# Optimization experiments

Hardware: AMD Instinct MI355X
Metric: run time of the kernel (lower is better)

The kernel has to match this reference:

```python
import jax, jax.numpy as jnp
import numpy as np

B, C, H, W = 8, 192, 128, 128
NH = 4  # num_heads
EPS = 1e-12


def setup_inputs() -> dict:
    key = jax.random.key(0)
    ks = jax.random.split(key, 10)
    s = 1.0 / np.sqrt(C)
    return {
        "x_q": jax.random.normal(ks[0], (B, C, H, W), jnp.float32),
        "x_k": jax.random.normal(ks[1], (B, C, H, W), jnp.float32),
        "Wq": jax.random.uniform(ks[2], (C, C), jnp.float32, -s, s),
        "bq": jax.random.uniform(ks[3], (C,), jnp.float32, -s, s),
        "Wkv": jax.random.uniform(ks[4], (2 * C, C), jnp.float32, -s, s),
        "bkv": jax.random.uniform(ks[5], (2 * C,), jnp.float32, -s, s),
        "Wp": jax.random.uniform(ks[6], (C, C), jnp.float32, -s, s),
        "bp": jax.random.uniform(ks[7], (C,), jnp.float32, -s, s),
        "temperature": jnp.ones((NH, 1, 1), jnp.float32),
    }


def _l2norm(x, axis):
    # torch F.normalize: x / clamp_min(||x||, eps)
    n = jnp.sqrt(jnp.sum(x * x, axis=axis, keepdims=True))
    return x / jnp.maximum(n, EPS)


def reference(x_q, x_k, Wq, bq, Wkv, bkv, Wp, bp, temperature):
    # 1x1 convs == channel matmuls
    q = jnp.einsum('oc,bchw->bohw', Wq, x_q) + bq[:, None, None]
    kv = jnp.einsum('oc,bchw->bohw', Wkv, x_k) + bkv[:, None, None]
    k, v = jnp.split(kv, 2, axis=1)

    def heads(t):  # (B,C,H,W) -> (B,NH,C//NH, H*W)
        return t.reshape(B, NH, C // NH, H * W)

    q, k, v = heads(q), heads(k), heads(v)
    q = _l2norm(q, 2)
    k = _l2norm(k, 2)

    attn_scale = 0.1 * jax.nn.sigmoid(temperature)  # (NH,1,1)
    attn = jnp.einsum('bhcd,bhkd->bhck', q, k) * attn_scale
    attn = jax.nn.softmax(attn, axis=-1)
    out = jnp.einsum('bhck,bhkd->bhcd', attn, v)
    out = out.reshape(B, C, H, W)
    out = jnp.einsum('oc,bchw->bohw', Wp, out) + bp[:, None, None]
    return out
```

## Files before the change

kernel.cpp:

```cpp
#include <hip/hip_runtime.h>
#include <hip/hip_bf16.h>

#define HW 16384
#define CC 192
#define BB 8
#define NHD 4
#define HD 48

typedef __attribute__((ext_vector_type(8))) short  short8;
typedef __attribute__((ext_vector_type(4))) float  f32x4;

static __device__ __forceinline__ unsigned short f2bf(float f) {
  unsigned u = __float_as_uint(f);
  u += 0x7fffu + ((u >> 16) & 1u);
  return (unsigned short)(u >> 16);
}
static __device__ __forceinline__ unsigned pk2bf(float lo, float hi) {
  __hip_bfloat162 h = __float22bfloat162_rn(make_float2(lo, hi));
  return *reinterpret_cast<unsigned*>(&h);
}

static __device__ __forceinline__ void ldsbar() {
  asm volatile("" ::: "memory");
  asm volatile("s_waitcnt lgkmcnt(0)" ::: "memory");
  __builtin_amdgcn_s_barrier();
  asm volatile("" ::: "memory");
}

__global__ __launch_bounds__(256) void cast_w_kernel(
    const float* __restrict__ Wq, const float* __restrict__ Wkv,
    unsigned short* __restrict__ Wb)
{
  const int i = blockIdx.x * 256 + threadIdx.x;
  const float v = (i < CC*CC) ? Wq[i] : Wkv[i - CC*CC];
  Wb[i] = f2bf(v);
}

__global__ __launch_bounds__(256, 2) void qkg_kernel(
    const float* __restrict__ x_q, const float* __restrict__ x_k,
    const unsigned short* __restrict__ wb,
    const float* __restrict__ bq, const float* __restrict__ bkv,
    float* __restrict__ gpart)
{
  const int tid  = threadIdx.x;
  const int lane = tid & 63;
  const int wv   = tid >> 6;
  const int b    = blockIdx.y;
  const int p0   = blockIdx.x * 256;
  const int l15  = lane & 15;
  const int lg   = lane >> 4;
  const int qd   = tid & 15;

  __shared__ unsigned short Xs[64][200];
  __shared__ unsigned short QN[NHD][48][68];
  __shared__ unsigned short KN[NHD][48][68];

  const float* Xq = x_q + (size_t)b*CC*HW;
  const float* Xk = x_k + (size_t)b*CC*HW;

  f32x4 pre[12];
  auto LOADT = [&](const float* X, int pb) {
    #pragma unroll
    for (int i = 0; i < 6; ++i) {
      const int cp = (tid >> 4) + i*16;
      const float* base = X + (size_t)(2*cp)*HW + pb + qd*4;
      pre[2*i]   = *(const f32x4*)(base);
      pre[2*i+1] = *(const f32x4*)(base + HW);
    }
  };
  auto WRITET = [&]() {
    #pragma unroll
    for (int i = 0; i < 6; ++i) {
      const int cp = (tid >> 4) + i*16;
      #pragma unroll
      for (int j = 0; j < 4; ++j)
        *(unsigned*)&Xs[qd*4 + j][2*cp] = pk2bf(pre[2*i][j], pre[2*i+1][j]);
    }
  };

  auto PROJ = [&](const unsigned short* W, const float* bias,
                  unsigned short (*DST)[68]) {
    f32x4 acc[3][4];
    #pragma unroll
    for (int mt = 0; mt < 3; ++mt)
      #pragma unroll
      for (int nt = 0; nt < 4; ++nt)
        acc[mt][nt] = (f32x4){0.f, 0.f, 0.f, 0.f};

    #pragma unroll
    for (int kk = 0; kk < 6; ++kk) {
      short8 afr[3], bfr[4];
      #pragma unroll
      for (int mt = 0; mt < 3; ++mt)
        afr[mt] = *(const short8*)(W + (size_t)(wv*48 + mt*16 + l15)*CC + kk*32 + lg*8);
      #pragma unroll
      for (int nt = 0; nt < 4; ++nt)
        bfr[nt] = *(const short8*)&Xs[nt*16 + l15][kk*32 + lg*8];
      #pragma unroll
      for (int mt = 0; mt < 3; ++mt)
        #pragma unroll
        for (int nt = 0; nt < 4; ++nt)
          acc[mt][nt] = __builtin_amdgcn_mfma_f32_16x16x32_bf16(
              afr[mt], bfr[nt], acc[mt][nt], 0, 0, 0);
    }

    #pragma unroll
    for (int nt = 0; nt < 4; ++nt) {
      float v[3][4];
      float ss = 0.f;
      #pragma unroll
      for (int mt = 0; mt < 3; ++mt)
        #pragma unroll
        for (int r = 0; r < 4; ++r) {
          const float x = acc[mt][nt][r] + bias[wv*48 + mt*16 + lg*4 + r];
          v[mt][r] = x;
          ss += x*x;
        }
      ss += __shfl_xor(ss, 16);
      ss += __shfl_xor(ss, 32);
      const float rn = 1.0f / fmaxf(sqrtf(ss), 1e-12f);
      #pragma unroll
      for (int mt = 0; mt < 3; ++mt)
        #pragma unroll
        for (int r = 0; r < 4; ++r)
          DST[mt*16 + lg*4 + r][nt*16 + l15] = f2bf(v[mt][r] * rn);
    }
  };

  f32x4 gacc[3][3];
  #pragma unroll
  for (int mt = 0; mt < 3; ++mt)
    #pragma unroll
    for (int nt = 0; nt < 3; ++nt)
      gacc[mt][nt] = (f32x4){0.f, 0.f, 0.f, 0.f};

  LOADT(Xq, p0);
  for (int t = 0; t < 4; ++t) {
    const int pb = p0 + t*64;
    WRITET();
    ldsbar();
    LOADT(Xk, pb);
    PROJ(wb, bq, QN[wv]);
    ldsbar();
    WRITET();
    ldsbar();
    if (t < 3) LOADT(Xq, pb + 64);
    PROJ(wb + (size_t)CC*CC, bkv, KN[wv]);
    ldsbar();

    #pragma unroll
    for (int s = 0; s < 2; ++s) {
      short8 ga[3], gb[3];
      #pragma unroll
      for (int mt = 0; mt < 3; ++mt)
        ga[mt] = *(const short8*)&QN[wv][mt*16 + l15][s*32 + lg*8];
      #pragma unroll
      for (int nt = 0; nt < 3; ++nt)
        gb[nt] = *(const short8*)&KN[wv][nt*16 + l15][s*32 + lg*8];
      #pragma unroll
      for (int mt = 0; mt < 3; ++mt)
        #pragma unroll
        for (int nt = 0; nt < 3; ++nt)
          gacc[mt][nt] = __builtin_amdgcn_mfma_f32_16x16x32_bf16(
              ga[mt], gb[nt], gacc[mt][nt], 0, 0, 0);
    }
  }

  float* G = gpart + ((size_t)(b*NHD + wv)*64 + blockIdx.x)*2304;
  #pragma unroll
  for (int mt = 0; mt < 3; ++mt)
    #pragma unroll
    for (int nt = 0; nt < 3; ++nt)
      #pragma unroll
      for (int r = 0; r < 4; ++r)
        G[(mt*16 + lg*4 + r)*HD + nt*16 + l15] = gacc[mt][nt][r];
}

__global__ __launch_bounds__(256) void proj_fin(
    const float* __restrict__ x_k,
    const unsigned short* __restrict__ w3b,
    const float* __restrict__ b3,
    float* __restrict__ of)
{
  const int tid  = threadIdx.x;
  const int lane = tid & 63;
  const int wv   = tid >> 6;
  const int b    = blockIdx.y;
  const int p0   = blockIdx.x * 256;
  const int l15  = lane & 15;
  const int lg   = lane >> 4;
  const int qd   = tid & 15;

  __shared__ unsigned short Xt[2][64][200];

  const float* X = x_k + (size_t)b*CC*HW;
  const unsigned short* Wb = w3b + (size_t)b*CC*CC;
  const float* bias = b3 + (size_t)b*CC;

  short8 afr[6][3];
  #pragma unroll
  for (int kk = 0; kk < 6; ++kk)
    #pragma unroll
    for (int mt = 0; mt < 3; ++mt)
      afr[kk][mt] = *(const short8*)(Wb + (size_t)(wv*48 + mt*16 + l15)*CC + kk*32 + lg*8);

  float bv[3][4];
  #pragma unroll
  for (int mt = 0; mt < 3; ++mt)
    #pragma unroll
    for (int r = 0; r < 4; ++r)
      bv[mt][r] = bias[wv*48 + mt*16 + lg*4 + r];

  f32x4 pre[12];
  auto LOADT = [&](int pb) {
    #pragma unroll
    for (int i = 0; i < 6; ++i) {
      const int cp = (tid >> 4) + i*16;
      const float* base = X + (size_t)(2*cp)*HW + pb + qd*4;
      pre[2*i]   = *(const f32x4*)(base);
      pre[2*i+1] = *(const f32x4*)(base + HW);
    }
  };
  auto WRITET = [&](int buf) {
    #pragma unroll
    for (int i = 0; i < 6; ++i) {
      const int cp = (tid >> 4) + i*16;
      #pragma unroll
      for (int j = 0; j < 4; ++j)
        *(unsigned*)&Xt[buf][qd*4 + j][2*cp] = pk2bf(pre[2*i][j], pre[2*i+1][j]);
    }
  };

  float* Ofp = of + (size_t)b*CC*HW;

  auto COMPUTE = [&](int buf, int pb) {
    f32x4 acc[3][4];
    #pragma unroll
    for (int mt = 0; mt < 3; ++mt)
      #pragma unroll
      for (int nt = 0; nt < 4; ++nt)
        acc[mt][nt] = (f32x4){0.f, 0.f, 0.f, 0.f};

    #pragma unroll
    for (int kk = 0; kk < 6; ++kk) {
      short8 bfr[4];
      #pragma unroll
      for (int nt = 0; nt < 4; ++nt)
        bfr[nt] = *(const short8*)&Xt[buf][nt*16 + l15][kk*32 + lg*8];
      #pragma unroll
      for (int mt = 0; mt < 3; ++mt)
        #pragma unroll
        for (int nt = 0; nt < 4; ++nt)
          acc[mt][nt] = __builtin_amdgcn_mfma_f32_16x16x32_bf16(
              afr[kk][mt], bfr[nt], acc[mt][nt], 0, 0, 0);
    }

    #pragma unroll
    for (int nt = 0; nt < 4; ++nt) {
      const int col = pb + nt*16 + l15;
      #pragma unroll
      for (int mt = 0; mt < 3; ++mt)
        #pragma unroll
        for (int r = 0; r < 4; ++r)
          Ofp[(size_t)(wv*48 + mt*16 + lg*4 + r)*HW + col] = acc[mt][nt][r] + bv[mt][r];
    }
  };

  LOADT(p0);
  WRITET(0);
  ldsbar();
  #pragma unroll
  for (int t = 0; t < 4; ++t) {
    if (t < 3) LOADT(p0 + (t+1)*64);
    COMPUTE(t & 1, p0 + t*64);
    if (t < 3) {
      WRITET((t & 1) ^ 1);
      ldsbar();
    }
  }
}

__global__ __launch_bounds__(256) void attn_m_kernel(
    const float* __restrict__ Gpart,
    const float* __restrict__ Wp,
    const float* __restrict__ temp,
    float* __restrict__ Mf)
{
  __shared__ float att[HD][52];
  const int bh  = blockIdx.x;
  const int b   = bh >> 2, h = bh & 3;
  const int tid = threadIdx.x;
  const float* src = Gpart + (size_t)bh*64*2304;

  #pragma unroll
  for (int i = 0; i < 9; ++i) {
    const int e = tid + i*256;
    float s = 0.f;
    #pragma unroll
    for (int k = 0; k < 64; ++k) s += src[(size_t)k*2304 + e];
    att[e/48][e%48] = s;
  }
  __syncthreads();

  const int g = tid >> 2, sl = tid & 3;
  if (g < HD) {
    const float t = temp[h];
    const float scale = 0.1f / (1.0f + expf(-t));
    float* row = att[g];
    float m = -1e30f;
    #pragma unroll
    for (int jj = 0; jj < 12; ++jj) m = fmaxf(m, row[sl + jj*4]);
    m = fmaxf(m, __shfl_xor(m, 1));
    m = fmaxf(m, __shfl_xor(m, 2));
    float ev[12];
    float s = 0.f;
    #pragma unroll
    for (int jj = 0; jj < 12; ++jj) {
      const float e = expf((row[sl + jj*4] - m) * scale);
      ev[jj] = e; s += e;
    }
    s += __shfl_xor(s, 1);
    s += __shfl_xor(s, 2);
    const float inv = 1.0f / s;
    #pragma unroll
    for (int jj = 0; jj < 12; ++jj) row[sl + jj*4] = ev[jj] * inv;
  }
  __syncthreads();

  #pragma unroll
  for (int i = 0; i < 36; ++i) {
    const int idx = tid + i*256;
    const int o = idx / HD, k2 = idx % HD;
    const float* wrow = Wp + (size_t)o*CC + h*HD;
    float s = 0.f;
    #pragma unroll
    for (int c = 0; c < HD; ++c) s += wrow[c] * att[c][k2];
    Mf[(size_t)b*CC*CC + (size_t)o*CC + h*HD + k2] = s;
  }
}

__global__ __launch_bounds__(192) void w3_kernel(
    const float* __restrict__ Mf, const float* __restrict__ Wkv,
    const float* __restrict__ bkv, const float* __restrict__ bp,
    unsigned short* __restrict__ W3b, float* __restrict__ b3)
{
  const int b  = blockIdx.x;
  const int o0 = blockIdx.y * 8;
  const int j  = threadIdx.x;
  const float* M  = Mf + ((size_t)b*CC + o0)*CC;
  const float* Wv = Wkv + (size_t)CC*CC;
  const float* bv = bkv + CC;

  float acc[8]  = {0.f,0.f,0.f,0.f,0.f,0.f,0.f,0.f};
  float bacc[8] = {0.f,0.f,0.f,0.f,0.f,0.f,0.f,0.f};
  #pragma unroll 4
  for (int k = 0; k < CC; ++k) {
    const float w  = Wv[(size_t)k*CC + j];
    const float bk = bv[k];
    #pragma unroll
    for (int r = 0; r < 8; ++r) {
      const float m = M[r*CC + k];
      acc[r]  += m * w;
      bacc[r] += m * bk;
    }
  }
  unsigned short* dst = W3b + ((size_t)b*CC + o0)*CC + j;
  #pragma unroll
  for (int r = 0; r < 8; ++r) dst[(size_t)r*CC] = f2bf(acc[r]);
  if (j < 8) b3[(size_t)b*CC + o0 + j] = bacc[j] + bp[o0 + j];
}

extern "C" void kernel_launch(void* const* d_in, const int* in_sizes, int n_in,
                              void* d_out, int out_size, void* d_ws, size_t ws_size,
                              hipStream_t stream)
{
  (void)in_sizes; (void)n_in; (void)out_size; (void)ws_size;
  const float* x_q  = (const float*)d_in[0];
  const float* x_k  = (const float*)d_in[1];
  const float* Wq   = (const float*)d_in[2];
  const float* bq   = (const float*)d_in[3];
  const float* Wkv  = (const float*)d_in[4];
  const float* bkv  = (const float*)d_in[5];
  const float* Wp   = (const float*)d_in[6];
  const float* bp   = (const float*)d_in[7];
  const float* temp = (const float*)d_in[8];

  char* p = (char*)d_ws;
  float* gpart = (float*)p;                 p += (size_t)BB*NHD*64*2304*sizeof(float);
  float* mf = (float*)p;                    p += (size_t)BB*CC*CC*sizeof(float);
  unsigned short* w3b = (unsigned short*)p; p += (size_t)BB*CC*CC*sizeof(unsigned short);
  float* b3 = (float*)p;                    p += (size_t)BB*CC*sizeof(float);
  unsigned short* wb = (unsigned short*)p;

  cast_w_kernel<<<dim3((2*CC*CC)/256), 256, 0, stream>>>(Wq, Wkv, wb);

  qkg_kernel<<<dim3(HW/256, BB), 256, 0, stream>>>(
      x_q, x_k, wb, bq, bkv, gpart);

  attn_m_kernel<<<dim3(BB*NHD), 256, 0, stream>>>(gpart, Wp, temp, mf);
  w3_kernel<<<dim3(BB, 24), 192, 0, stream>>>(mf, Wkv, bkv, bp, w3b, b3);

  proj_fin<<<dim3(HW/256, BB), 256, 0, stream>>>(x_k, w3b, b3, (float*)d_out);
}
```

Baseline: 170.4 us.

## Split qkg into smaller 128-pixel blocks with joint q/k staging and fewer barriers

The Gram-partial kernel now processes 128 pixels per block in 32-pixel chunks instead of 256 in 64-pixel chunks. This doubles the grid and raises the occupancy hint to 3. Each chunk loads and stages x_q and x_k together into separate LDS buffers, cutting barriers from four to two per iteration and shrinking LDS use. In exchange, the partial Gram buffer doubles and the reduction in attn_m_kernel sums 128 partials per element, which adds memory traffic and serial work in that single small kernel.

```diff
diff --git a/kernel.cpp b/kernel.cpp
--- a/kernel.cpp
+++ b/kernel.cpp
@@ -36,11 +36,151 @@
   Wb[i] = f2bf(v);
 }
 
-__global__ __launch_bounds__(256, 2) void qkg_kernel(
+__global__ __launch_bounds__(256, 3) void qkg_kernel(
     const float* __restrict__ x_q, const float* __restrict__ x_k,
     const unsigned short* __restrict__ wb,
     const float* __restrict__ bq, const float* __restrict__ bkv,
     float* __restrict__ gpart)
+{
+  const int tid  = threadIdx.x;
+  const int lane = tid & 63;
+  const int wv   = tid >> 6;
+  const int b    = blockIdx.y;
+  const int p0   = blockIdx.x * 128;
+  const int l15  = lane & 15;
+  const int lg   = lane >> 4;
+
+  __shared__ unsigned short Xsq[32][200];
+  __shared__ unsigned short Xsk[32][200];
+  __shared__ unsigned short QN[NHD][48][34];
+  __shared__ unsigned short KN[NHD][48][34];
+
+  const float* Xq = x_q + (size_t)b*CC*HW;
+  const float* Xk = x_k + (size_t)b*CC*HW;
+
+  f32x4 pre[12];
+  auto LOADT2 = [&](int pb) {
+    #pragma unroll
+    for (int i = 0; i < 3; ++i) {
+      const int it = tid + i*256;
+      const int qd = it & 7, cp = it >> 3;
+      const float* bq_ = Xq + (size_t)(2*cp)*HW + pb + qd*4;
+      const float* bk_ = Xk + (size_t)(2*cp)*HW + pb + qd*4;
+      pre[2*i]     = *(const f32x4*)(bq_);
+      pre[2*i + 1] = *(const f32x4*)(bq_ + HW);
+      pre[6 + 2*i]     = *(const f32x4*)(bk_);
+      pre[6 + 2*i + 1] = *(const f32x4*)(bk_ + HW);
+    }
+  };
+  auto WRITET2 = [&]() {
+    #pragma unroll
+    for (int i = 0; i < 3; ++i) {
+      const int it = tid + i*256;
+      const int qd = it & 7, cp = it >> 3;
+      #pragma unroll
+      for (int j = 0; j < 4; ++j) {
+        *(unsigned*)&Xsq[qd*4 + j][2*cp] = pk2bf(pre[2*i][j], pre[2*i+1][j]);
+        *(unsigned*)&Xsk[qd*4 + j][2*cp] = pk2bf(pre[6+2*i][j], pre[6+2*i+1][j]);
+      }
+    }
+  };
+
+  auto PROJ32 = [&](const unsigned short* W, const float* bias,
+                    unsigned short (*SRC)[200], unsigned short (*DST)[34]) {
+    f32x4 acc[3][2];
+    #pragma unroll
+    for (int mt = 0; mt < 3; ++mt)
+      #pragma unroll
+      for (int nt = 0; nt < 2; ++nt)
+        acc[mt][nt] = (f32x4){0.f, 0.f, 0.f, 0.f};
+
+    #pragma unroll
+    for (int kk = 0; kk < 6; ++kk) {
+      short8 afr[3], bfr[2];
+      #pragma unroll
+      for (int mt = 0; mt < 3; ++mt)
+        afr[mt] = *(const short8*)(W + (size_t)(wv*48 + mt*16 + l15)*CC + kk*32 + lg*8);
+      #pragma unroll
+      for (int nt = 0; nt < 2; ++nt)
+        bfr[nt] = *(const short8*)&SRC[nt*16 + l15][kk*32 + lg*8];
+      #pragma unroll
+      for (int mt = 0; mt < 3; ++mt)
+        #pragma unroll
+        for (int nt = 0; nt < 2; ++nt)
+          acc[mt][nt] = __builtin_amdgcn_mfma_f32_16x16x32_bf16(
+              afr[mt], bfr[nt], acc[mt][nt], 0, 0, 0);
+    }
+
+    #pragma unroll
+    for (int nt = 0; nt < 2; ++nt) {
+      float v[3][4];
+      float ss = 0.f;
+      #pragma unroll
+      for (int mt = 0; mt < 3; ++mt)
+        #pragma unroll
+        for (int r = 0; r < 4; ++r) {
+          const float x = acc[mt][nt][r] + bias[wv*48 + mt*16 + lg*4 + r];
+          v[mt][r] = x;
+          ss += x*x;
+        }
+      ss += __shfl_xor(ss, 16);
+      ss += __shfl_xor(ss, 32);
+      const float rn = 1.0f / fmaxf(sqrtf(ss), 1e-12f);
+      #pragma unroll
+      for (int mt = 0; mt < 3; ++mt)
+        #pragma unroll
+        for (int r = 0; r < 4; ++r)
+          DST[mt*16 + lg*4 + r][nt*16 + l15] = f2bf(v[mt][r] * rn);
+    }
+  };
+
+  f32x4 gacc[3][3];
+  #pragma unroll
+  for (int mt = 0; mt < 3; ++mt)
+    #pragma unroll
+    for (int nt = 0; nt < 3; ++nt)
+      gacc[mt][nt] = (f32x4){0.f, 0.f, 0.f, 0.f};
+
+  LOADT2(p0);
+  for (int t = 0; t < 4; ++t) {
+    WRITET2();
+    ldsbar();
+    if (t < 3) LOADT2(p0 + (t+1)*32);
+    PROJ32(wb, bq, Xsq, QN[wv]);
+    PROJ32(wb + (size_t)CC*CC, bkv, Xsk, KN[wv]);
+    {
+      short8 ga[3], gb[3];
+      #pragma unroll
+      for (int mt = 0; mt < 3; ++mt)
+        ga[mt] = *(const short8*)&QN[wv][mt*16 + l15][lg*8];
+      #pragma unroll
+      for (int nt = 0; nt < 3; ++nt)
+        gb[nt] = *(const short8*)&KN[wv][nt*16 + l15][lg*8];
+      #pragma unroll
+      for (int mt = 0; mt < 3; ++mt)
+        #pragma unroll
+        for (int nt = 0; nt < 3; ++nt)
+          gacc[mt][nt] = __builtin_amdgcn_mfma_f32_16x16x32_bf16(
+              ga[mt], gb[nt], gacc[mt][nt], 0, 0, 0);
+    }
+    ldsbar();
+  }
+
+  float* G = gpart + ((size_t)(b*NHD + wv)*128 + blockIdx.x)*2304;
+  #pragma unroll
+  for (int mt = 0; mt < 3; ++mt)
+    #pragma unroll
+    for (int nt = 0; nt < 3; ++nt)
+      #pragma unroll
+      for (int r = 0; r < 4; ++r)
+        G[(mt*16 + lg*4 + r)*HD + nt*16 + l15] = gacc[mt][nt][r];
+}
+
+__global__ __launch_bounds__(256) void proj_fin(
+    const float* __restrict__ x_k,
+    const unsigned short* __restrict__ w3b,
+    const float* __restrict__ b3,
+    float* __restrict__ of)
 {
   const int tid  = threadIdx.x;
   const int lane = tid & 63;
@@ -51,146 +191,6 @@
   const int lg   = lane >> 4;
   const int qd   = tid & 15;
 
-  __shared__ unsigned short Xs[64][200];
-  __shared__ unsigned short QN[NHD][48][68];
-  __shared__ unsigned short KN[NHD][48][68];
-
-  const float* Xq = x_q + (size_t)b*CC*HW;
-  const float* Xk = x_k + (size_t)b*CC*HW;
-
-  f32x4 pre[12];
-  auto LOADT = [&](const float* X, int pb) {
-    #pragma unroll
-    for (int i = 0; i < 6; ++i) {
-      const int cp = (tid >> 4) + i*16;
-      const float* base = X + (size_t)(2*cp)*HW + pb + qd*4;
-      pre[2*i]   = *(const f32x4*)(base);
-      pre[2*i+1] = *(const f32x4*)(base + HW);
-    }
-  };
-  auto WRITET = [&]() {
-    #pragma unroll
-    for (int i = 0; i < 6; ++i) {
-      const int cp = (tid >> 4) + i*16;
-      #pragma unroll
-      for (int j = 0; j < 4; ++j)
-        *(unsigned*)&Xs[qd*4 + j][2*cp] = pk2bf(pre[2*i][j], pre[2*i+1][j]);
-    }
-  };
-
-  auto PROJ = [&](const unsigned short* W, const float* bias,
-                  unsigned short (*DST)[68]) {
-    f32x4 acc[3][4];
-    #pragma unroll
-    for (int mt = 0; mt < 3; ++mt)
-      #pragma unroll
-      for (int nt = 0; nt < 4; ++nt)
-        acc[mt][nt] = (f32x4){0.f, 0.f, 0.f, 0.f};
-
-    #pragma unroll
-    for (int kk = 0; kk < 6; ++kk) {
-      short8 afr[3], bfr[4];
-      #pragma unroll
-      for (int mt = 0; mt < 3; ++mt)
-        afr[mt] = *(const short8*)(W + (size_t)(wv*48 + mt*16 + l15)*CC + kk*32 + lg*8);
-      #pragma unroll
-      for (int nt = 0; nt < 4; ++nt)
-        bfr[nt] = *(const short8*)&Xs[nt*16 + l15][kk*32 + lg*8];
-      #pragma unroll
-      for (int mt = 0; mt < 3; ++mt)
-        #pragma unroll
-        for (int nt = 0; nt < 4; ++nt)
-          acc[mt][nt] = __builtin_amdgcn_mfma_f32_16x16x32_bf16(
-              afr[mt], bfr[nt], acc[mt][nt], 0, 0, 0);
-    }
-
-    #pragma unroll
-    for (int nt = 0; nt < 4; ++nt) {
-      float v[3][4];
-      float ss = 0.f;
-      #pragma unroll
-      for (int mt = 0; mt < 3; ++mt)
-        #pragma unroll
-        for (int r = 0; r < 4; ++r) {
-          const float x = acc[mt][nt][r] + bias[wv*48 + mt*16 + lg*4 + r];
-          v[mt][r] = x;
-          ss += x*x;
-        }
-      ss += __shfl_xor(ss, 16);
-      ss += __shfl_xor(ss, 32);
-      const float rn = 1.0f / fmaxf(sqrtf(ss), 1e-12f);
-      #pragma unroll
-      for (int mt = 0; mt < 3; ++mt)
-        #pragma unroll
-        for (int r = 0; r < 4; ++r)
-          DST[mt*16 + lg*4 + r][nt*16 + l15] = f2bf(v[mt][r] * rn);
-    }
-  };
-
-  f32x4 gacc[3][3];
-  #pragma unroll
-  for (int mt = 0; mt < 3; ++mt)
-    #pragma unroll
-    for (int nt = 0; nt < 3; ++nt)
-      gacc[mt][nt] = (f32x4){0.f, 0.f, 0.f, 0.f};
-
-  LOADT(Xq, p0);
-  for (int t = 0; t < 4; ++t) {
-    const int pb = p0 + t*64;
-    WRITET();
-    ldsbar();
-    LOADT(Xk, pb);
-    PROJ(wb, bq, QN[wv]);
-    ldsbar();
-    WRITET();
-    ldsbar();
-    if (t < 3) LOADT(Xq, pb + 64);
-    PROJ(wb + (size_t)CC*CC, bkv, KN[wv]);
-    ldsbar();
-
-    #pragma unroll
-    for (int s = 0; s < 2; ++s) {
-      short8 ga[3], gb[3];
-      #pragma unroll
-      for (int mt = 0; mt < 3; ++mt)
-        ga[mt] = *(const short8*)&QN[wv][mt*16 + l15][s*32 + lg*8];
-      #pragma unroll
-      for (int nt = 0; nt < 3; ++nt)
-        gb[nt] = *(const short8*)&KN[wv][nt*16 + l15][s*32 + lg*8];
-      #pragma unroll
-      for (int mt = 0; mt < 3; ++mt)
-        #pragma unroll
-        for (int nt = 0; nt < 3; ++nt)
-          gacc[mt][nt] = __builtin_amdgcn_mfma_f32_16x16x32_bf16(
-              ga[mt], gb[nt], gacc[mt][nt], 0, 0, 0);
-    }
-  }
-
-  float* G = gpart + ((size_t)(b*NHD + wv)*64 + blockIdx.x)*2304;
-  #pragma unroll
-  for (int mt = 0; mt < 3; ++mt)
-    #pragma unroll
-    for (int nt = 0; nt < 3; ++nt)
-      #pragma unroll
-      for (int r = 0; r < 4; ++r)
-        G[(mt*16 + lg*4 + r)*HD + nt*16 + l15] = gacc[mt][nt][r];
-}
-
-__global__ __launch_bounds__(256) void proj_fin(
-    const float* __restrict__ x_k,
-    const unsigned short* __restrict__ w3b,
-    const float* __restrict__ b3,
-    float* __restrict__ of)
-{
-  const int tid  = threadIdx.x;
-  const int lane = tid & 63;
-  const int wv   = tid >> 6;
-  const int b    = blockIdx.y;
-  const int p0   = blockIdx.x * 256;
-  const int l15  = lane & 15;
-  const int lg   = lane >> 4;
-  const int qd   = tid & 15;
-
   __shared__ unsigned short Xt[2][64][200];
 
   const float* X = x_k + (size_t)b*CC*HW;
@@ -290,14 +290,13 @@
   const int bh  = blockIdx.x;
   const int b   = bh >> 2, h = bh & 3;
   const int tid = threadIdx.x;
-  const float* src = Gpart + (size_t)bh*64*2304;
+  const float* src = Gpart + (size_t)bh*128*2304;
 
   #pragma unroll
   for (int i = 0; i < 9; ++i) {
     const int e = tid + i*256;
     float s = 0.f;
-    #pragma unroll
-    for (int k = 0; k < 64; ++k) s += src[(size_t)k*2304 + e];
+    for (int k = 0; k < 128; ++k) s += src[(size_t)k*2304 + e];
     att[e/48][e%48] = s;
   }
   __syncthreads();
@@ -386,7 +385,7 @@
   const float* temp = (const float*)d_in[8];
 
   char* p = (char*)d_ws;
-  float* gpart = (float*)p;                 p += (size_t)BB*NHD*64*2304*sizeof(float);
+  float* gpart = (float*)p;                 p += (size_t)BB*NHD*128*2304*sizeof(float);
   float* mf = (float*)p;                    p += (size_t)BB*CC*CC*sizeof(float);
   unsigned short* w3b = (unsigned short*)p; p += (size_t)BB*CC*CC*sizeof(unsigned short);
   float* b3 = (float*)p;                    p += (size_t)BB*CC*sizeof(float);
@@ -394,7 +393,7 @@
 
   cast_w_kernel<<<dim3((2*CC*CC)/256), 256, 0, stream>>>(Wq, Wkv, wb);
 
-  qkg_kernel<<<dim3(HW/256, BB), 256, 0, stream>>>(
+  qkg_kernel<<<dim3(HW/128, BB), 256, 0, stream>>>(
       x_q, x_k, wb, bq, bkv, gpart);
 
   attn_m_kernel<<<dim3(BB*NHD), 256, 0, stream>>>(gpart, Wp, temp, mf);
```

New measurement: 325.9 us. +91.3%, slower.
